# Performance work log

Measured on AMD Instinct MI355X. Metric: run time of the kernel, lower is better.

The kernel has to match this reference:

```python
import jax, jax.numpy as jnp
import numpy as np

DIM = 1024
NUM_HEADS = 16
HEAD_DIM = DIM // NUM_HEADS
SCALE = HEAD_DIM ** -0.5


def setup_inputs() -> dict:
    key = jax.random.key(0)
    k1, k2, k3 = jax.random.split(key, 3)
    B, N = 2, 2048
    x = jax.random.normal(k1, (B, N, DIM), dtype=jnp.float32)
    w_qkv = jax.random.normal(k2, (3 * DIM, DIM), dtype=jnp.float32) * (DIM ** -0.5)
    w_proj = jax.random.normal(k3, (DIM, DIM), dtype=jnp.float32) * (DIM ** -0.5)
    b_proj = jnp.zeros((DIM,), dtype=jnp.float32)
    return {"x": x, "w_qkv": w_qkv, "w_proj": w_proj, "b_proj": b_proj}


def reference(x, w_qkv, w_proj, b_proj):
    B, N, C = x.shape
    # qkv projection (no bias): [B,N,3C] -> [3,B,H,N,Dh]
    qkv = jnp.einsum('bnc,dc->bnd', x, w_qkv)
    qkv = qkv.reshape(B, N, 3, NUM_HEADS, HEAD_DIM).transpose(2, 0, 3, 1, 4)
    q, k, v = qkv[0], qkv[1], qkv[2]
    # scaled dot-product attention (full score matrix, as in source)
    attn = jnp.einsum('bhnd,bhmd->bhnm', q * SCALE, k)
    attn = jax.nn.softmax(attn, axis=-1)
    out = jnp.einsum('bhnm,bhmd->bhnd', attn, v)  # [B,H,N,Dh]
    out = out.transpose(0, 2, 1, 3).reshape(B, N, C)
    return out @ w_proj.T + b_proj
```

## Files before the change

kernel.cpp:

```cpp
#include <hip/hip_runtime.h>

#define DIM   1024
#define NH    16
#define HD    64
#define BATCH 2
#define SEQ   2048
#define MTOT  4096
#define SCALE 0.125f
#define LOG2E 1.44269504088896340736f

typedef __attribute__((ext_vector_type(8))) _Float16 half8_t;
typedef __attribute__((ext_vector_type(4))) _Float16 half4_t;
typedef __attribute__((ext_vector_type(2))) __fp16 pk16x2_t;
typedef __attribute__((ext_vector_type(4))) float f32x4;

union H4 { pk16x2_t h2[2]; half4_t h4; ushort4 us; };

__device__ __forceinline__ float4 ld4(const float* p) { return *(const float4*)p; }

__device__ __forceinline__ unsigned short f2h(float f) {
    _Float16 h = (_Float16)f;
    return *(unsigned short*)&h;
}

__device__ __forceinline__ float fast_exp2(float x) {
#if __has_builtin(__builtin_amdgcn_exp2f)
    return __builtin_amdgcn_exp2f(x);
#else
    return exp2f(x);
#endif
}

__device__ __forceinline__ void gl2lds16(const void* g, void* l) {
    __builtin_amdgcn_global_load_lds(
        (const __attribute__((address_space(1))) unsigned int*)g,
        (__attribute__((address_space(3))) unsigned int*)l, 16, 0, 0);
}

__global__ __launch_bounds__(256) void cvt3(const float* __restrict__ x,
                                            const float* __restrict__ wq,
                                            const float* __restrict__ wp,
                                            unsigned short* __restrict__ xh,
                                            unsigned short* __restrict__ wqh,
                                            unsigned short* __restrict__ wph) {
    size_t i = ((size_t)blockIdx.x * 256 + threadIdx.x) * 4;
    if (i < (size_t)MTOT * DIM) {
        float4 t = ld4(x + i);
        ushort4 o = {f2h(t.x), f2h(t.y), f2h(t.z), f2h(t.w)};
        *(ushort4*)(xh + i) = o;
    }
    if (i < (size_t)3 * DIM * DIM) {
        float4 t = ld4(wq + i);
        ushort4 o = {f2h(t.x), f2h(t.y), f2h(t.z), f2h(t.w)};
        *(ushort4*)(wqh + i) = o;
    }
    if (i < (size_t)DIM * DIM) {
        float4 t = ld4(wp + i);
        ushort4 o = {f2h(t.x), f2h(t.y), f2h(t.z), f2h(t.w)};
        *(ushort4*)(wph + i) = o;
    }
}

__device__ __forceinline__ void gemm128_core(const unsigned short* __restrict__ A,
                                             const unsigned short* __restrict__ B,
                                             int m0, int n0, int K,
                                             unsigned short* As, unsigned short* Bs,
                                             f32x4 acc[4][4]) {
    const int tid  = threadIdx.x;
    const int w    = tid >> 6;
    const int lane = tid & 63;
    const int g = lane >> 4, c = lane & 15;
    const int wr = w >> 1, wc = w & 1;

    const int lr = lane >> 3;
    const int js = lane & 7;
    const int j0 = js ^ lr;
    const unsigned short* gA = A + (size_t)(m0 + w * 32 + lr) * K + j0 * 8;
    const unsigned short* gB = B + (size_t)(n0 + w * 32 + lr) * K + j0 * 8;
    unsigned short* lA = As + w * 32 * 64;
    unsigned short* lB = Bs + w * 32 * 64;

    int aoff[4], boff[4];
    #pragma unroll
    for (int t = 0; t < 4; ++t) {
        aoff[t] = (wr * 64 + t * 16 + c) * 64 + ((g ^ (c & 7)) * 8);
        boff[t] = (wc * 64 + t * 16 + c) * 64 + ((g ^ (c & 7)) * 8);
    }

    for (int kb = 0; kb < K; kb += 64) {
        if (kb) __syncthreads();
        #pragma unroll
        for (int i = 0; i < 4; ++i) {
            gl2lds16(gA + kb + (size_t)(8 * i) * K, lA + i * 512);
            gl2lds16(gB + kb + (size_t)(8 * i) * K, lB + i * 512);
        }
        __syncthreads();
        half8_t af0[4], af1[4], bf0[4], bf1[4];
        #pragma unroll
        for (int t = 0; t < 4; ++t) {
            af0[t] = *(const half8_t*)&As[aoff[t]];
            af1[t] = *(const half8_t*)&As[aoff[t] ^ 32];
            bf0[t] = *(const half8_t*)&Bs[boff[t]];
            bf1[t] = *(const half8_t*)&Bs[boff[t] ^ 32];
        }
        #pragma unroll
        for (int rt = 0; rt < 4; ++rt)
            #pragma unroll
            for (int ct = 0; ct < 4; ++ct)
                acc[rt][ct] = __builtin_amdgcn_mfma_f32_16x16x32_f16(
                    af0[rt], bf0[ct], acc[rt][ct], 0, 0, 0);
        #pragma unroll
        for (int rt = 0; rt < 4; ++rt)
            #pragma unroll
            for (int ct = 0; ct < 4; ++ct)
                acc[rt][ct] = __builtin_amdgcn_mfma_f32_16x16x32_f16(
                    af1[rt], bf1[ct], acc[rt][ct], 0, 0, 0);
    }
}

__global__ __launch_bounds__(256) void qkv_mfma(const unsigned short* __restrict__ xh,
                                                const unsigned short* __restrict__ wqh,
                                                unsigned short* __restrict__ q,
                                                unsigned short* __restrict__ k,
                                                unsigned short* __restrict__ vt) {
    __shared__ unsigned short As[128 * 64];
    __shared__ unsigned short Bs[128 * 64];
    const int m0 = blockIdx.x * 128;
    const int n0 = blockIdx.y * 128;
    f32x4 acc[4][4];
    #pragma unroll
    for (int i = 0; i < 4; ++i)
        #pragma unroll
        for (int jj = 0; jj < 4; ++jj) acc[i][jj] = (f32x4){0.f, 0.f, 0.f, 0.f};

    gemm128_core(xh, wqh, m0, n0, DIM, As, Bs, acc);

    const int tid = threadIdx.x, w = tid >> 6, lane = tid & 63;
    const int g = lane >> 4, c = lane & 15;
    const int wr = w >> 1, wc = w & 1;
    const int which = n0 >> 10;
    const int hh    = ((n0 + wc * 64) & 1023) >> 6;
    const int b     = m0 >> 11;
    const int nb    = m0 & 2047;

    if (which == 2) {
        unsigned short* base = vt + (size_t)(b * NH + hh) * HD * SEQ;
        #pragma unroll
        for (int rt = 0; rt < 4; ++rt)
            #pragma unroll
            for (int ct = 0; ct < 4; ++ct) {
                int n4 = nb + wr * 64 + rt * 16 + 4 * g;
                H4 u;
                u.h2[0] = __builtin_amdgcn_cvt_pkrtz(acc[rt][ct][0], acc[rt][ct][1]);
                u.h2[1] = __builtin_amdgcn_cvt_pkrtz(acc[rt][ct][2], acc[rt][ct][3]);
                *(ushort4*)&base[(size_t)(ct * 16 + c) * SEQ + n4] = u.us;
            }
    } else {
        unsigned short* dst  = (which == 0) ? q : k;
        unsigned short* base = dst + (size_t)(b * NH + hh) * SEQ * HD;
        const float sc = (which == 0) ? SCALE * LOG2E : 1.0f;
        #pragma unroll
        for (int rt = 0; rt < 4; ++rt)
            #pragma unroll
            for (int ct = 0; ct < 4; ++ct)
                #pragma unroll
                for (int r = 0; r < 4; ++r) {
                    int row = nb + wr * 64 + rt * 16 + g * 4 + r;
                    base[(size_t)row * HD + ct * 16 + c] = f2h(acc[rt][ct][r] * sc);
                }
    }
}

__global__ __launch_bounds__(256) void proj_mfma(const unsigned short* __restrict__ aoh,
                                                 const unsigned short* __restrict__ wph,
                                                 const float* __restrict__ bias,
                                                 float* __restrict__ out) {
    __shared__ unsigned short As[64 * 64];
    __shared__ unsigned short Bs[128 * 64];
    const int m0 = blockIdx.x * 64;
    const int n0 = blockIdx.y * 128;
    const int tid = threadIdx.x, w = tid >> 6, lane = tid & 63;
    const int g = lane >> 4, c = lane & 15;
    const int wm = w & 1, wn = w >> 1;

    f32x4 acc[2][4];
    #pragma unroll
    for (int i = 0; i < 2; ++i)
        #pragma unroll
        for (int jj = 0; jj < 4; ++jj) acc[i][jj] = (f32x4){0.f, 0.f, 0.f, 0.f};

    const int lr = lane >> 3, js = lane & 7, j0 = js ^ lr;
    const unsigned short* gA = aoh + (size_t)(m0 + w * 16 + lr) * DIM + j0 * 8;
    const unsigned short* gB = wph + (size_t)(n0 + w * 32 + lr) * DIM + j0 * 8;
    unsigned short* lA = As + w * 16 * 64;
    unsigned short* lB = Bs + w * 32 * 64;

    int aoff[2], boff[4];
    #pragma unroll
    for (int t = 0; t < 2; ++t)
        aoff[t] = (wm * 32 + t * 16 + c) * 64 + ((g ^ (c & 7)) * 8);
    #pragma unroll
    for (int t = 0; t < 4; ++t)
        boff[t] = (wn * 64 + t * 16 + c) * 64 + ((g ^ (c & 7)) * 8);

    for (int kb = 0; kb < DIM; kb += 64) {
        if (kb) __syncthreads();
        #pragma unroll
        for (int i = 0; i < 2; ++i)
            gl2lds16(gA + kb + (size_t)(8 * i) * DIM, lA + i * 512);
        #pragma unroll
        for (int i = 0; i < 4; ++i)
            gl2lds16(gB + kb + (size_t)(8 * i) * DIM, lB + i * 512);
        __syncthreads();
        half8_t af0[2], af1[2], bf0[4], bf1[4];
        #pragma unroll
        for (int t = 0; t < 2; ++t) {
            af0[t] = *(const half8_t*)&As[aoff[t]];
            af1[t] = *(const half8_t*)&As[aoff[t] ^ 32];
        }
        #pragma unroll
        for (int t = 0; t < 4; ++t) {
            bf0[t] = *(const half8_t*)&Bs[boff[t]];
            bf1[t] = *(const half8_t*)&Bs[boff[t] ^ 32];
        }
        #pragma unroll
        for (int rt = 0; rt < 2; ++rt)
            #pragma unroll
            for (int ct = 0; ct < 4; ++ct) {
                acc[rt][ct] = __builtin_amdgcn_mfma_f32_16x16x32_f16(
                    af0[rt], bf0[ct], acc[rt][ct], 0, 0, 0);
                acc[rt][ct] = __builtin_amdgcn_mfma_f32_16x16x32_f16(
                    af1[rt], bf1[ct], acc[rt][ct], 0, 0, 0);
            }
    }

    float br[4];
    #pragma unroll
    for (int ct = 0; ct < 4; ++ct) br[ct] = bias[n0 + wn * 64 + ct * 16 + c];
    #pragma unroll
    for (int rt = 0; rt < 2; ++rt)
        #pragma unroll
        for (int ct = 0; ct < 4; ++ct)
            #pragma unroll
            for (int r = 0; r < 4; ++r) {
                int row = m0 + wm * 32 + rt * 16 + g * 4 + r;
                out[(size_t)row * DIM + n0 + wn * 64 + ct * 16 + c] =
                    acc[rt][ct][r] + br[ct];
            }
}

__global__ __launch_bounds__(256) void attn_mfma(const unsigned short* __restrict__ q,
                                                 const unsigned short* __restrict__ k,
                                                 const unsigned short* __restrict__ vt,
                                                 unsigned short* __restrict__ aoh) {
    __shared__ unsigned short Ks[128 * 64];
    __shared__ unsigned short Vs[64 * 128];

    const int tid  = threadIdx.x;
    const int w    = tid >> 6;
    const int lane = tid & 63;
    const int g    = lane >> 4;
    const int c    = lane & 15;
    const int id = blockIdx.x;
    const int qt = (id >> 3) & 15;
    const int bh = ((id >> 7) << 3) | (id & 7);
    const int b = bh >> 4, h = bh & 15;
    const int q0 = qt * 128 + w * 32;

    const unsigned short* qbase = q + ((size_t)bh * SEQ + q0) * HD;
    half8_t qf[2][2];
    #pragma unroll
    for (int s = 0; s < 2; ++s) {
        const unsigned short* qr = qbase + (size_t)(s * 16 + c) * HD + g * 8;
        qf[s][0] = *(const half8_t*)qr;
        qf[s][1] = *(const half8_t*)(qr + 32);
    }

    f32x4 o[2][4];
    #pragma unroll
    for (int s = 0; s < 2; ++s)
        #pragma unroll
        for (int dt = 0; dt < 4; ++dt) o[s][dt] = (f32x4){0.f, 0.f, 0.f, 0.f};
    float rs0 = 0.f, rs1 = 0.f;

    const int lr = lane >> 3, js = lane & 7, j0 = js ^ lr;
    const unsigned short* kg = k + (size_t)bh * SEQ * HD + (size_t)(w * 32 + lr) * HD + j0 * 8;
    unsigned short* lK = Ks + w * 32 * 64;
    const int vlr = lane >> 4, vjs = lane & 15;
    const unsigned short* vg[4];
    #pragma unroll
    for (int i = 0; i < 4; ++i)
        vg[i] = vt + (size_t)bh * HD * SEQ + (size_t)(w * 16 + 4 * i + vlr) * SEQ
                   + (vjs ^ (4 * i + vlr)) * 8;
    unsigned short* lV = Vs + w * 16 * 128;

    int koff[8];
    #pragma unroll
    for (int ct = 0; ct < 8; ++ct)
        koff[ct] = (ct * 16 + c) * 64 + ((g ^ (c & 7)) * 8);

    for (int kt = 0; kt < 16; ++kt) {
        if (kt) __syncthreads();
        const size_t kadv = (size_t)kt * 128 * HD;
        #pragma unroll
        for (int i = 0; i < 4; ++i) {
            gl2lds16(kg + kadv + (size_t)(8 * i) * HD, lK + i * 512);
            gl2lds16(vg[i] + kt * 128,                 lV + i * 512);
        }
        __syncthreads();

        half4_t pf0[8], pf1[8];
        #pragma unroll
        for (int ct = 0; ct < 8; ++ct) {
            half8_t kf0 = *(const half8_t*)&Ks[koff[ct]];
            half8_t kf1 = *(const half8_t*)&Ks[koff[ct] ^ 32];
            f32x4 s0 = __builtin_amdgcn_mfma_f32_16x16x32_f16(kf0, qf[0][0],
                           (f32x4){0.f, 0.f, 0.f, 0.f}, 0, 0, 0);
            s0 = __builtin_amdgcn_mfma_f32_16x16x32_f16(kf1, qf[0][1], s0, 0, 0, 0);
            f32x4 s1 = __builtin_amdgcn_mfma_f32_16x16x32_f16(kf0, qf[1][0],
                           (f32x4){0.f, 0.f, 0.f, 0.f}, 0, 0, 0);
            s1 = __builtin_amdgcn_mfma_f32_16x16x32_f16(kf1, qf[1][1], s1, 0, 0, 0);

            float a0 = fast_exp2(s0[0]), a1 = fast_exp2(s0[1]);
            float a2 = fast_exp2(s0[2]), a3 = fast_exp2(s0[3]);
            rs0 += (a0 + a1) + (a2 + a3);
            H4 u0; u0.h2[0] = __builtin_amdgcn_cvt_pkrtz(a0, a1);
                   u0.h2[1] = __builtin_amdgcn_cvt_pkrtz(a2, a3);
            pf0[ct] = u0.h4;
            float b0 = fast_exp2(s1[0]), b1 = fast_exp2(s1[1]);
            float b2 = fast_exp2(s1[2]), b3 = fast_exp2(s1[3]);
            rs1 += (b0 + b1) + (b2 + b3);
            H4 u1; u1.h2[0] = __builtin_amdgcn_cvt_pkrtz(b0, b1);
                   u1.h2[1] = __builtin_amdgcn_cvt_pkrtz(b2, b3);
            pf1[ct] = u1.h4;
        }

        #pragma unroll
        for (int dt = 0; dt < 4; ++dt) {
            #pragma unroll
            for (int kt2 = 0; kt2 < 8; ++kt2) {
                int voff = (dt * 16 + c) * 128 +
                           (((2 * kt2 + (g >> 1)) ^ c) * 8) + 4 * (g & 1);
                half4_t vf = *(const half4_t*)&Vs[voff];
                o[0][dt] = __builtin_amdgcn_mfma_f32_16x16x16f16(vf, pf0[kt2], o[0][dt], 0, 0, 0);
                o[1][dt] = __builtin_amdgcn_mfma_f32_16x16x16f16(vf, pf1[kt2], o[1][dt], 0, 0, 0);
            }
        }
    }

    rs0 += __shfl_xor(rs0, 16); rs0 += __shfl_xor(rs0, 32);
    rs1 += __shfl_xor(rs1, 16); rs1 += __shfl_xor(rs1, 32);
    const float inv[2] = {1.0f / rs0, 1.0f / rs1};

    #pragma unroll
    for (int s = 0; s < 2; ++s) {
        unsigned short* orow = aoh + ((size_t)b * SEQ + q0 + s * 16 + c) * DIM + h * HD;
        #pragma unroll
        for (int dt = 0; dt < 4; ++dt) {
            H4 u;
            u.h2[0] = __builtin_amdgcn_cvt_pkrtz(o[s][dt][0] * inv[s], o[s][dt][1] * inv[s]);
            u.h2[1] = __builtin_amdgcn_cvt_pkrtz(o[s][dt][2] * inv[s], o[s][dt][3] * inv[s]);
            *(ushort4*)&orow[dt * 16 + 4 * g] = u.us;
        }
    }
}

extern "C" void kernel_launch(void* const* d_in, const int* in_sizes, int n_in,
                              void* d_out, int out_size, void* d_ws, size_t ws_size,
                              hipStream_t stream) {
    const float* x      = (const float*)d_in[0];
    const float* w_qkv  = (const float*)d_in[1];
    const float* w_proj = (const float*)d_in[2];
    const float* b_proj = (const float*)d_in[3];
    float* out = (float*)d_out;

    const size_t per = (size_t)BATCH * NH * SEQ * HD;
    const size_t nwq = (size_t)3 * DIM * DIM;
    const size_t nwp = (size_t)DIM * DIM;
    const size_t need = (5 * per + nwq + nwp) * sizeof(unsigned short);
    if (ws_size < need) return;

    unsigned short* q   = (unsigned short*)d_ws;
    unsigned short* k   = q + per;
    unsigned short* vt  = k + per;
    unsigned short* aoh = vt + per;
    unsigned short* xh  = aoh + per;
    unsigned short* wqh = xh + per;
    unsigned short* wph = wqh + nwq;

    cvt3<<<dim3(4096), 256, 0, stream>>>(x, w_qkv, w_proj, xh, wqh, wph);
    qkv_mfma<<<dim3(32, 24), 256, 0, stream>>>(xh, wqh, q, k, vt);
    attn_mfma<<<dim3(512), 256, 0, stream>>>(q, k, vt, aoh);
    proj_mfma<<<dim3(64, 8), 256, 0, stream>>>(aoh, wph, b_proj, out);
}
```

Before: 170.2 us.

## Use 8 waves per attention block and XCD-aware tile mapping for QKV GEMM

```diff
diff --git a/kernel.cpp b/kernel.cpp
--- a/kernel.cpp
+++ b/kernel.cpp
@@ -125,8 +125,11 @@
                                                 unsigned short* __restrict__ vt) {
     __shared__ unsigned short As[128 * 64];
     __shared__ unsigned short Bs[128 * 64];
-    const int m0 = blockIdx.x * 128;
-    const int n0 = blockIdx.y * 128;
+    const int id = blockIdx.x;
+    const int xcd = id & 7;
+    const int j  = id >> 3;
+    const int m0 = (((xcd & 3) * 8) + (j & 7)) * 128;
+    const int n0 = (((xcd >> 2) * 12) + (j >> 3)) * 128;
     f32x4 acc[4][4];
     #pragma unroll
     for (int i = 0; i < 4; ++i)
@@ -249,7 +252,7 @@
             }
 }
 
-__global__ __launch_bounds__(256) void attn_mfma(const unsigned short* __restrict__ q,
+__global__ __launch_bounds__(512) void attn_mfma(const unsigned short* __restrict__ q,
                                                  const unsigned short* __restrict__ k,
                                                  const unsigned short* __restrict__ vt,
                                                  unsigned short* __restrict__ aoh) {
@@ -265,34 +268,28 @@
     const int qt = (id >> 3) & 15;
     const int bh = ((id >> 7) << 3) | (id & 7);
     const int b = bh >> 4, h = bh & 15;
-    const int q0 = qt * 128 + w * 32;
-
-    const unsigned short* qbase = q + ((size_t)bh * SEQ + q0) * HD;
-    half8_t qf[2][2];
-    #pragma unroll
-    for (int s = 0; s < 2; ++s) {
-        const unsigned short* qr = qbase + (size_t)(s * 16 + c) * HD + g * 8;
-        qf[s][0] = *(const half8_t*)qr;
-        qf[s][1] = *(const half8_t*)(qr + 32);
-    }
-
-    f32x4 o[2][4];
-    #pragma unroll
-    for (int s = 0; s < 2; ++s)
-        #pragma unroll
-        for (int dt = 0; dt < 4; ++dt) o[s][dt] = (f32x4){0.f, 0.f, 0.f, 0.f};
-    float rs0 = 0.f, rs1 = 0.f;
+    const int q0 = qt * 128 + w * 16;
+
+    const unsigned short* qr = q + ((size_t)bh * SEQ + q0 + c) * HD + g * 8;
+    half8_t qf0 = *(const half8_t*)qr;
+    half8_t qf1 = *(const half8_t*)(qr + 32);
+
+    f32x4 o[4];
+    #pragma unroll
+    for (int dt = 0; dt < 4; ++dt) o[dt] = (f32x4){0.f, 0.f, 0.f, 0.f};
+    float rs = 0.f;
 
     const int lr = lane >> 3, js = lane & 7, j0 = js ^ lr;
-    const unsigned short* kg = k + (size_t)bh * SEQ * HD + (size_t)(w * 32 + lr) * HD + j0 * 8;
-    unsigned short* lK = Ks + w * 32 * 64;
+    const unsigned short* kg = k + (size_t)bh * SEQ * HD + (size_t)(w * 16 + lr) * HD + j0 * 8;
+    unsigned short* lK = Ks + w * 16 * 64;
     const int vlr = lane >> 4, vjs = lane & 15;
-    const unsigned short* vg[4];
-    #pragma unroll
-    for (int i = 0; i < 4; ++i)
-        vg[i] = vt + (size_t)bh * HD * SEQ + (size_t)(w * 16 + 4 * i + vlr) * SEQ
-                   + (vjs ^ (4 * i + vlr)) * 8;
-    unsigned short* lV = Vs + w * 16 * 128;
+    const unsigned short* vg[2];
+    #pragma unroll
+    for (int i = 0; i < 2; ++i) {
+        int d = w * 8 + 4 * i + vlr;
+        vg[i] = vt + (size_t)bh * HD * SEQ + (size_t)d * SEQ + (vjs ^ (d & 15)) * 8;
+    }
+    unsigned short* lV = Vs + w * 8 * 128;
 
     int koff[8];
     #pragma unroll
@@ -302,37 +299,27 @@
     for (int kt = 0; kt < 16; ++kt) {
         if (kt) __syncthreads();
         const size_t kadv = (size_t)kt * 128 * HD;
-        #pragma unroll
-        for (int i = 0; i < 4; ++i) {
-            gl2lds16(kg + kadv + (size_t)(8 * i) * HD, lK + i * 512);
-            gl2lds16(vg[i] + kt * 128,                 lV + i * 512);
-        }
+        gl2lds16(kg + kadv,          lK);
+        gl2lds16(kg + kadv + 8 * HD, lK + 512);
+        gl2lds16(vg[0] + kt * 128,   lV);
+        gl2lds16(vg[1] + kt * 128,   lV + 512);
         __syncthreads();
 
-        half4_t pf0[8], pf1[8];
+        half4_t pf[8];
         #pragma unroll
         for (int ct = 0; ct < 8; ++ct) {
             half8_t kf0 = *(const half8_t*)&Ks[koff[ct]];
             half8_t kf1 = *(const half8_t*)&Ks[koff[ct] ^ 32];
-            f32x4 s0 = __builtin_amdgcn_mfma_f32_16x16x32_f16(kf0, qf[0][0],
+            f32x4 s0 = __builtin_amdgcn_mfma_f32_16x16x32_f16(kf0, qf0,
                            (f32x4){0.f, 0.f, 0.f, 0.f}, 0, 0, 0);
-            s0 = __builtin_amdgcn_mfma_f32_16x16x32_f16(kf1, qf[0][1], s0, 0, 0, 0);
-            f32x4 s1 = __builtin_amdgcn_mfma_f32_16x16x32_f16(kf0, qf[1][0],
-                           (f32x4){0.f, 0.f, 0.f, 0.f}, 0, 0, 0);
-            s1 = __builtin_amdgcn_mfma_f32_16x16x32_f16(kf1, qf[1][1], s1, 0, 0, 0);
+            s0 = __builtin_amdgcn_mfma_f32_16x16x32_f16(kf1, qf1, s0, 0, 0, 0);
 
             float a0 = fast_exp2(s0[0]), a1 = fast_exp2(s0[1]);
             float a2 = fast_exp2(s0[2]), a3 = fast_exp2(s0[3]);
-            rs0 += (a0 + a1) + (a2 + a3);
+            rs += (a0 + a1) + (a2 + a3);
             H4 u0; u0.h2[0] = __builtin_amdgcn_cvt_pkrtz(a0, a1);
                    u0.h2[1] = __builtin_amdgcn_cvt_pkrtz(a2, a3);
-            pf0[ct] = u0.h4;
-            float b0 = fast_exp2(s1[0]), b1 = fast_exp2(s1[1]);
-            float b2 = fast_exp2(s1[2]), b3 = fast_exp2(s1[3]);
-            rs1 += (b0 + b1) + (b2 + b3);
-            H4 u1; u1.h2[0] = __builtin_amdgcn_cvt_pkrtz(b0, b1);
-                   u1.h2[1] = __builtin_amdgcn_cvt_pkrtz(b2, b3);
-            pf1[ct] = u1.h4;
+            pf[ct] = u0.h4;
         }
 
         #pragma unroll
@@ -342,26 +329,21 @@
                 int voff = (dt * 16 + c) * 128 +
                            (((2 * kt2 + (g >> 1)) ^ c) * 8) + 4 * (g & 1);
                 half4_t vf = *(const half4_t*)&Vs[voff];
-                o[0][dt] = __builtin_amdgcn_mfma_f32_16x16x16f16(vf, pf0[kt2], o[0][dt], 0, 0, 0);
-                o[1][dt] = __builtin_amdgcn_mfma_f32_16x16x16f16(vf, pf1[kt2], o[1][dt], 0, 0, 0);
+                o[dt] = __builtin_amdgcn_mfma_f32_16x16x16f16(vf, pf[kt2], o[dt], 0, 0, 0);
             }
         }
     }
 
-    rs0 += __shfl_xor(rs0, 16); rs0 += __shfl_xor(rs0, 32);
-    rs1 += __shfl_xor(rs1, 16); rs1 += __shfl_xor(rs1, 32);
-    const float inv[2] = {1.0f / rs0, 1.0f / rs1};
-
-    #pragma unroll
-    for (int s = 0; s < 2; ++s) {
-        unsigned short* orow = aoh + ((size_t)b * SEQ + q0 + s * 16 + c) * DIM + h * HD;
-        #pragma unroll
-        for (int dt = 0; dt < 4; ++dt) {
-            H4 u;
-            u.h2[0] = __builtin_amdgcn_cvt_pkrtz(o[s][dt][0] * inv[s], o[s][dt][1] * inv[s]);
-            u.h2[1] = __builtin_amdgcn_cvt_pkrtz(o[s][dt][2] * inv[s], o[s][dt][3] * inv[s]);
-            *(ushort4*)&orow[dt * 16 + 4 * g] = u.us;
-        }
+    rs += __shfl_xor(rs, 16); rs += __shfl_xor(rs, 32);
+    const float inv = 1.0f / rs;
+
+    unsigned short* orow = aoh + ((size_t)b * SEQ + q0 + c) * DIM + h * HD;
+    #pragma unroll
+    for (int dt = 0; dt < 4; ++dt) {
+        H4 u;
+        u.h2[0] = __builtin_amdgcn_cvt_pkrtz(o[dt][0] * inv, o[dt][1] * inv);
+        u.h2[1] = __builtin_amdgcn_cvt_pkrtz(o[dt][2] * inv, o[dt][3] * inv);
+        *(ushort4*)&orow[dt * 16 + 4 * g] = u.us;
     }
 }
 
@@ -389,7 +371,7 @@
     unsigned short* wph = wqh + nwq;
 
     cvt3<<<dim3(4096), 256, 0, stream>>>(x, w_qkv, w_proj, xh, wqh, wph);
-    qkv_mfma<<<dim3(32, 24), 256, 0, stream>>>(xh, wqh, q, k, vt);
-    attn_mfma<<<dim3(512), 256, 0, stream>>>(q, k, vt, aoh);
+    qkv_mfma<<<dim3(768), 256, 0, stream>>>(xh, wqh, q, k, vt);
+    attn_mfma<<<dim3(512), 512, 0, stream>>>(q, k, vt, aoh);
     proj_mfma<<<dim3(64, 8), 256, 0, stream>>>(aoh, wph, b_proj, out);
 }
```

New measurement: 179.1 us. 5.2% more time.
